# Optimization experiments

Hardware: AMD Instinct MI355X
Metric: run time of the kernel (lower is better)

The kernel has to match this reference:

```python
import jax, jax.numpy as jnp
import numpy as np

FACTOR = 1.0   # module's self.factor
EPS = 1e-6     # rmsnorm eps


def setup_inputs() -> dict:
    key = jax.random.key(0)
    k0, k1, k2, k3 = jax.random.split(key, 4)
    B, S = 4, 2048
    D_IN = D_STATE = D_OUT = 2048
    N_HEADS = 32
    HD = D_STATE // N_HEADS  # 64
    x = jax.random.normal(k0, (B, S, D_IN), jnp.float32)
    w_in = jax.random.normal(k1, (D_STATE, D_IN), jnp.float32) * 0.02
    b_in = jnp.zeros((D_STATE,), jnp.float32)
    state_weight = jax.random.normal(k2, (N_HEADS, HD, HD), jnp.float32) * 0.02
    norm_weight = jnp.ones((D_STATE,), jnp.float32)
    w_out = jax.random.normal(k3, (D_OUT, D_STATE), jnp.float32) * (0.02 / np.sqrt(2 * 24))
    return dict(x=x, w_in=w_in, b_in=b_in, state_weight=state_weight,
                norm_weight=norm_weight, w_out=w_out)


def _rnn_scan(xt, W):
    # xt: (B, S, N, H); W: (N, H, H)
    B, S, N, H = xt.shape

    def step(s, x_t):
        # s: (B, N, H) ; per-head linear recurrence with tanh nonlinearity
        s = jnp.tanh(jnp.einsum('bnh,nhk->bnk', s, W) + x_t)
        return s, s

    s0 = jnp.zeros((B, N, H), xt.dtype)
    _, states = jax.lax.scan(step, s0, jnp.swapaxes(xt, 0, 1))  # (S, B, N, H)
    return jnp.swapaxes(states, 0, 1)  # (B, S, N, H)


def reference(x, w_in, b_in, state_weight, norm_weight, w_out):
    B, S, _ = x.shape
    N, H, _ = state_weight.shape
    h = x @ w_in.T + b_in                      # input_projection: (B,S,state)
    h = h.reshape(B, S, N, H) * FACTOR
    W = state_weight * FACTOR
    states = _rnn_scan(h, W)                   # (B,S,N,H)
    y = states.reshape(B, S, N * H)
    # rmsnorm
    y = y * jax.lax.rsqrt(jnp.mean(y * y, axis=-1, keepdims=True) + EPS) * norm_weight
    return y @ w_out.T                         # output_projection (no bias)
```

## Files before the change

### kernel.cpp

```cpp
#include <hip/hip_runtime.h>
#include <hip/hip_bf16.h>
#include <cstdint>


typedef short bf16x8 __attribute__((ext_vector_type(8)));
typedef float f32x4 __attribute__((ext_vector_type(4)));
typedef _Float16 f16x2 __attribute__((ext_vector_type(2)));

#define GLD16(gp, lp)                                                          \
  __builtin_amdgcn_global_load_lds(                                            \
      (const __attribute__((address_space(1))) void*)(gp),                     \
      (__attribute__((address_space(3))) void*)(lp), 16, 0, 0)

__global__ __launch_bounds__(256) void cvt_f32_bf16(
    const float* __restrict__ in, __hip_bfloat16* __restrict__ out, int n4) {
  int i = blockIdx.x * 256 + threadIdx.x;
  if (i >= n4) return;
  float4 v = ((const float4*)in)[i];
  __hip_bfloat16 a = __float2bfloat16(v.x);
  __hip_bfloat16 b = __float2bfloat16(v.y);
  __hip_bfloat16 c = __float2bfloat16(v.z);
  __hip_bfloat16 d = __float2bfloat16(v.w);
  ushort4 p;
  p.x = *(unsigned short*)&a; p.y = *(unsigned short*)&b;
  p.z = *(unsigned short*)&c; p.w = *(unsigned short*)&d;
  ((ushort4*)out)[i] = p;
}

__global__ __launch_bounds__(256) void gemm_nt(
    const __hip_bfloat16* __restrict__ A, const __hip_bfloat16* __restrict__ B,
    const float* __restrict__ bias, float* __restrict__ C,
    int M, int N, int K) {
  __shared__ __hip_bfloat16 As[128 * 32];
  __shared__ __hip_bfloat16 Bs[128 * 32];
  const int tid  = threadIdx.x;
  const int lane = tid & 63;
  const int wave = tid >> 6;
  const int wm = wave >> 1, wn = wave & 1;

  const int id = blockIdx.y * gridDim.x + blockIdx.x;
  const int chunk = (gridDim.x * gridDim.y) >> 3;
  const int v = (id & 7) * chunk + (id >> 3);
  const int vbn = v / gridDim.y;
  const int vbm = v - vbn * gridDim.y;
  const long bm = (long)vbm * 128;
  const long bn = (long)vbn * 128;

  const int c0 = tid, c1 = tid + 256;
  const int r0 = c0 >> 2, k0 = (c0 & 3) * 8;
  const int r1 = c1 >> 2, k1 = (c1 & 3) * 8;
  __hip_bfloat16* lA0 = &As[(wave * 64) * 8];
  __hip_bfloat16* lA1 = &As[(256 + wave * 64) * 8];
  __hip_bfloat16* lB0 = &Bs[(wave * 64) * 8];
  __hip_bfloat16* lB1 = &Bs[(256 + wave * 64) * 8];
  const __hip_bfloat16* gA0 = A + (bm + r0) * (long)K + k0;
  const __hip_bfloat16* gA1 = A + (bm + r1) * (long)K + k1;
  const __hip_bfloat16* gB0 = B + (bn + r0) * (long)K + k0;
  const __hip_bfloat16* gB1 = B + (bn + r1) * (long)K + k1;

  const int fr = lane & 15;
  const int fk = (lane >> 4) * 8;

  f32x4 acc[4][4];
#pragma unroll
  for (int i = 0; i < 4; i++)
#pragma unroll
    for (int j = 0; j < 4; j++) acc[i][j] = {0.f, 0.f, 0.f, 0.f};

  for (int kt = 0; kt < K; kt += 32) {
    __syncthreads();
    GLD16(gA0 + kt, lA0);
    GLD16(gA1 + kt, lA1);
    GLD16(gB0 + kt, lB0);
    GLD16(gB1 + kt, lB1);
    __syncthreads();
    bf16x8 af[4], bfr[4];
#pragma unroll
    for (int t = 0; t < 4; t++)
      af[t] = *(const bf16x8*)&As[(wm * 64 + t * 16 + fr) * 32 + fk];
#pragma unroll
    for (int t = 0; t < 4; t++)
      bfr[t] = *(const bf16x8*)&Bs[(wn * 64 + t * 16 + fr) * 32 + fk];
#pragma unroll
    for (int i = 0; i < 4; i++)
#pragma unroll
      for (int j = 0; j < 4; j++)
        acc[i][j] = __builtin_amdgcn_mfma_f32_16x16x32_bf16(
            af[i], bfr[j], acc[i][j], 0, 0, 0);
  }

  const int cr = (lane >> 4) * 4;
  const int cc = lane & 15;
#pragma unroll
  for (int j = 0; j < 4; j++) {
    const long n = bn + wn * 64 + j * 16 + cc;
    const float bv = bias ? bias[n] : 0.0f;
#pragma unroll
    for (int i = 0; i < 4; i++) {
      const long m = bm + wm * 64 + i * 16 + cr;
#pragma unroll
      for (int r = 0; r < 4; r++)
        C[(m + r) * (long)N + n] = acc[i][j][r] + bv;
    }
  }
}

__device__ __forceinline__ float tanh_fast(float z) {
  float e = __builtin_amdgcn_exp2f(z * 2.8853900817779268f);
  return 1.0f - 2.0f * __builtin_amdgcn_rcpf(e + 1.0f);
}

__global__ __launch_bounds__(64) void scan_kernel(
    const float* __restrict__ Wst, float* __restrict__ h) {
  const int b = blockIdx.x >> 5;
  const int n = blockIdx.x & 31;
  const int lane = threadIdx.x;
  const float* Wn = Wst + n * 4096;

  f16x2 w2[32];
#pragma unroll
  for (int p = 0; p < 32; p++) {
    f16x2 t;
    t.x = (_Float16)Wn[(2 * p) * 64 + lane];
    t.y = (_Float16)Wn[(2 * p + 1) * 64 + lane];
    w2[p] = t;
  }

  __shared__ alignas(16) unsigned short s_h[64];

  int4 sv[8];
#pragma unroll
  for (int q = 0; q < 8; q++) sv[q] = make_int4(0, 0, 0, 0);

  float* hp = h + ((size_t)b * 2048) * 2048 + n * 64 + lane;
  float xcur[8], xnxt[8];
#pragma unroll
  for (int i = 0; i < 8; i++) xcur[i] = hp[(size_t)i * 2048];

  const f16x2 z2 = {(_Float16)0.f, (_Float16)0.f};

  for (int t0 = 0; t0 < 2048; t0 += 8) {
    if (t0 + 8 < 2048) {
#pragma unroll
      for (int i = 0; i < 8; i++)
        xnxt[i] = hp[(size_t)(t0 + 8 + i) * 2048];
    }
#pragma unroll
    for (int i = 0; i < 8; i++) {
      f16x2 ac0 = z2, ac1 = z2, ac2 = z2, ac3 = z2;
#pragma unroll
      for (int q = 0; q < 8; q++) {
        ac0 = __builtin_elementwise_fma(__builtin_bit_cast(f16x2, sv[q].x),
                                        w2[4 * q + 0], ac0);
        ac1 = __builtin_elementwise_fma(__builtin_bit_cast(f16x2, sv[q].y),
                                        w2[4 * q + 1], ac1);
        ac2 = __builtin_elementwise_fma(__builtin_bit_cast(f16x2, sv[q].z),
                                        w2[4 * q + 2], ac2);
        ac3 = __builtin_elementwise_fma(__builtin_bit_cast(f16x2, sv[q].w),
                                        w2[4 * q + 3], ac3);
      }
      f16x2 p01 = ac0 + ac1;
      f16x2 p23 = ac2 + ac3;
      f16x2 pt = p01 + p23;
      float z = (float)pt.x + (float)pt.y + xcur[i];
      float sn = tanh_fast(z);
      _Float16 sh = (_Float16)sn;
      s_h[lane] = __builtin_bit_cast(unsigned short, sh);
#pragma unroll
      for (int q = 0; q < 8; q++) sv[q] = ((const int4*)s_h)[q];
      hp[(size_t)(t0 + i) * 2048] = sn;
    }
#pragma unroll
    for (int i = 0; i < 8; i++) xcur[i] = xnxt[i];
  }
}

__global__ __launch_bounds__(256) void rmsnorm_to_bf16(
    const float* __restrict__ Y, const float* __restrict__ g,
    __hip_bfloat16* __restrict__ O) {
  const long row = blockIdx.x;
  const float* yr = Y + row * 2048;
  const int tid = threadIdx.x;
  float4 v0 = ((const float4*)yr)[tid * 2];
  float4 v1 = ((const float4*)yr)[tid * 2 + 1];
  float ss = v0.x * v0.x + v0.y * v0.y + v0.z * v0.z + v0.w * v0.w +
             v1.x * v1.x + v1.y * v1.y + v1.z * v1.z + v1.w * v1.w;
#pragma unroll
  for (int off = 32; off > 0; off >>= 1) ss += __shfl_down(ss, off);
  __shared__ float red[4];
  if ((tid & 63) == 0) red[tid >> 6] = ss;
  __syncthreads();
  float inv = rsqrtf((red[0] + red[1] + red[2] + red[3]) * (1.0f / 2048.0f)
                     + 1e-6f);
  float4 g0 = ((const float4*)(g + tid * 8))[0];
  float4 g1 = ((const float4*)(g + tid * 8))[1];
  float ov[8] = {v0.x * inv * g0.x, v0.y * inv * g0.y,
                 v0.z * inv * g0.z, v0.w * inv * g0.w,
                 v1.x * inv * g1.x, v1.y * inv * g1.y,
                 v1.z * inv * g1.z, v1.w * inv * g1.w};
  ushort4 p0, p1;
  __hip_bfloat16 t;
  t = __float2bfloat16(ov[0]); p0.x = *(unsigned short*)&t;
  t = __float2bfloat16(ov[1]); p0.y = *(unsigned short*)&t;
  t = __float2bfloat16(ov[2]); p0.z = *(unsigned short*)&t;
  t = __float2bfloat16(ov[3]); p0.w = *(unsigned short*)&t;
  t = __float2bfloat16(ov[4]); p1.x = *(unsigned short*)&t;
  t = __float2bfloat16(ov[5]); p1.y = *(unsigned short*)&t;
  t = __float2bfloat16(ov[6]); p1.z = *(unsigned short*)&t;
  t = __float2bfloat16(ov[7]); p1.w = *(unsigned short*)&t;
  ushort4* op = (ushort4*)(O + row * 2048 + tid * 8);
  op[0] = p0;
  op[1] = p1;
}

extern "C" void kernel_launch(void* const* d_in, const int* in_sizes, int n_in,
                              void* d_out, int out_size, void* d_ws,
                              size_t ws_size, hipStream_t stream) {
  const float* x     = (const float*)d_in[0];
  const float* w_in  = (const float*)d_in[1];
  const float* b_in  = (const float*)d_in[2];
  const float* w_st  = (const float*)d_in[3];
  const float* nw    = (const float*)d_in[4];
  const float* w_out = (const float*)d_in[5];
  float* out = (float*)d_out;

  char* ws = (char*)d_ws;
  __hip_bfloat16* x_bf  = (__hip_bfloat16*)(ws);
  __hip_bfloat16* wi_bf = (__hip_bfloat16*)(ws + 33554432);
  __hip_bfloat16* wo_bf = (__hip_bfloat16*)(ws + 41943040);
  float* h              = (float*)(ws + 50331648);

  cvt_f32_bf16<<<16384, 256, 0, stream>>>(x, x_bf, 4194304);
  cvt_f32_bf16<<<4096, 256, 0, stream>>>(w_in, wi_bf, 1048576);
  cvt_f32_bf16<<<4096, 256, 0, stream>>>(w_out, wo_bf, 1048576);

  gemm_nt<<<dim3(16, 64), 256, 0, stream>>>(x_bf, wi_bf, b_in, h,
                                            8192, 2048, 2048);
  scan_kernel<<<128, 64, 0, stream>>>(w_st, h);
  rmsnorm_to_bf16<<<8192, 256, 0, stream>>>(h, nw, x_bf);
  gemm_nt<<<dim3(16, 64), 256, 0, stream>>>(x_bf, wo_bf, nullptr, out,
                                            8192, 2048, 2048);
}
```

Baseline: 759.9 us.

## Use 256x256 GEMM tiles with double-buffered LDS and 512-thread blocks

Enlarges the GEMM block tile to 256x256 with eight waves, each computing a 128x64 sub-tile, which raises operand reuse per LDS load. It also adds a two-stage LDS buffer so the next K-slice is prefetched while MFMAs run on the current one. The grouped block-index swizzle is removed, and the grid shrinks to 256 blocks, which may reduce L2 locality and occupancy. Register pressure rises with 128 accumulator registers per lane.

```diff
diff --git a/kernel.cpp b/kernel.cpp
--- a/kernel.cpp
+++ b/kernel.cpp
@@ -27,67 +27,69 @@
   ((ushort4*)out)[i] = p;
 }
 
-__global__ __launch_bounds__(256) void gemm_nt(
+__global__ __launch_bounds__(512) void gemm_nt(
     const __hip_bfloat16* __restrict__ A, const __hip_bfloat16* __restrict__ B,
     const float* __restrict__ bias, float* __restrict__ C,
     int M, int N, int K) {
-  __shared__ __hip_bfloat16 As[128 * 32];
-  __shared__ __hip_bfloat16 Bs[128 * 32];
+  __shared__ __hip_bfloat16 As[2][256 * 32];
+  __shared__ __hip_bfloat16 Bs[2][256 * 32];
   const int tid  = threadIdx.x;
   const int lane = tid & 63;
   const int wave = tid >> 6;
-  const int wm = wave >> 1, wn = wave & 1;
-
-  const int id = blockIdx.y * gridDim.x + blockIdx.x;
-  const int chunk = (gridDim.x * gridDim.y) >> 3;
-  const int v = (id & 7) * chunk + (id >> 3);
-  const int vbn = v / gridDim.y;
-  const int vbm = v - vbn * gridDim.y;
-  const long bm = (long)vbm * 128;
-  const long bn = (long)vbn * 128;
-
-  const int c0 = tid, c1 = tid + 256;
-  const int r0 = c0 >> 2, k0 = (c0 & 3) * 8;
-  const int r1 = c1 >> 2, k1 = (c1 & 3) * 8;
-  __hip_bfloat16* lA0 = &As[(wave * 64) * 8];
-  __hip_bfloat16* lA1 = &As[(256 + wave * 64) * 8];
-  __hip_bfloat16* lB0 = &Bs[(wave * 64) * 8];
-  __hip_bfloat16* lB1 = &Bs[(256 + wave * 64) * 8];
+  const int wm = wave >> 2;
+  const int wn = wave & 3;
+  const long bm = (long)blockIdx.y * 256;
+  const long bn = (long)blockIdx.x * 256;
+
+  const int r0 = tid >> 2;
+  const int k0 = (tid & 3) * 8;
   const __hip_bfloat16* gA0 = A + (bm + r0) * (long)K + k0;
-  const __hip_bfloat16* gA1 = A + (bm + r1) * (long)K + k1;
+  const __hip_bfloat16* gA1 = A + (bm + 128 + r0) * (long)K + k0;
   const __hip_bfloat16* gB0 = B + (bn + r0) * (long)K + k0;
-  const __hip_bfloat16* gB1 = B + (bn + r1) * (long)K + k1;
+  const __hip_bfloat16* gB1 = B + (bn + 128 + r0) * (long)K + k0;
+
+#define STAGE(sbuf, kt)                                                        \
+  do {                                                                         \
+    GLD16(gA0 + (kt) * 32, &As[sbuf][wave * 512]);                             \
+    GLD16(gA1 + (kt) * 32, &As[sbuf][4096 + wave * 512]);                      \
+    GLD16(gB0 + (kt) * 32, &Bs[sbuf][wave * 512]);                             \
+    GLD16(gB1 + (kt) * 32, &Bs[sbuf][4096 + wave * 512]);                      \
+  } while (0)
 
   const int fr = lane & 15;
   const int fk = (lane >> 4) * 8;
 
-  f32x4 acc[4][4];
-#pragma unroll
-  for (int i = 0; i < 4; i++)
+  f32x4 acc[8][4];
+#pragma unroll
+  for (int i = 0; i < 8; i++)
 #pragma unroll
     for (int j = 0; j < 4; j++) acc[i][j] = {0.f, 0.f, 0.f, 0.f};
 
-  for (int kt = 0; kt < K; kt += 32) {
-    __syncthreads();
-    GLD16(gA0 + kt, lA0);
-    GLD16(gA1 + kt, lA1);
-    GLD16(gB0 + kt, lB0);
-    GLD16(gB1 + kt, lB1);
-    __syncthreads();
-    bf16x8 af[4], bfr[4];
+  STAGE(0, 0);
+  asm volatile("s_waitcnt vmcnt(0)" ::: "memory");
+  __syncthreads();
+
+  const int nk = K >> 5;
+  for (int kt = 0; kt < nk; kt++) {
+    const int cur = kt & 1;
+    if (kt + 1 < nk) STAGE(cur ^ 1, kt + 1);
+    bf16x8 af[8], bfr[4];
+#pragma unroll
+    for (int t = 0; t < 8; t++)
+      af[t] = *(const bf16x8*)&As[cur][(wm * 128 + t * 16 + fr) * 32 + fk];
 #pragma unroll
     for (int t = 0; t < 4; t++)
-      af[t] = *(const bf16x8*)&As[(wm * 64 + t * 16 + fr) * 32 + fk];
-#pragma unroll
-    for (int t = 0; t < 4; t++)
-      bfr[t] = *(const bf16x8*)&Bs[(wn * 64 + t * 16 + fr) * 32 + fk];
-#pragma unroll
-    for (int i = 0; i < 4; i++)
+      bfr[t] = *(const bf16x8*)&Bs[cur][(wn * 64 + t * 16 + fr) * 32 + fk];
+#pragma unroll
+    for (int i = 0; i < 8; i++)
 #pragma unroll
       for (int j = 0; j < 4; j++)
         acc[i][j] = __builtin_amdgcn_mfma_f32_16x16x32_bf16(
             af[i], bfr[j], acc[i][j], 0, 0, 0);
-  }
+    asm volatile("s_waitcnt vmcnt(0)" ::: "memory");
+    __syncthreads();
+  }
+#undef STAGE
 
   const int cr = (lane >> 4) * 4;
   const int cc = lane & 15;
@@ -96,8 +98,8 @@
     const long n = bn + wn * 64 + j * 16 + cc;
     const float bv = bias ? bias[n] : 0.0f;
 #pragma unroll
-    for (int i = 0; i < 4; i++) {
-      const long m = bm + wm * 64 + i * 16 + cr;
+    for (int i = 0; i < 8; i++) {
+      const long m = bm + wm * 128 + i * 16 + cr;
 #pragma unroll
       for (int r = 0; r < 4; r++)
         C[(m + r) * (long)N + n] = acc[i][j][r] + bv;
@@ -234,10 +236,10 @@
   cvt_f32_bf16<<<4096, 256, 0, stream>>>(w_in, wi_bf, 1048576);
   cvt_f32_bf16<<<4096, 256, 0, stream>>>(w_out, wo_bf, 1048576);
 
-  gemm_nt<<<dim3(16, 64), 256, 0, stream>>>(x_bf, wi_bf, b_in, h,
-                                            8192, 2048, 2048);
+  gemm_nt<<<dim3(8, 32), 512, 0, stream>>>(x_bf, wi_bf, b_in, h,
+                                           8192, 2048, 2048);
   scan_kernel<<<128, 64, 0, stream>>>(w_st, h);
   rmsnorm_to_bf16<<<8192, 256, 0, stream>>>(h, nw, x_bf);
-  gemm_nt<<<dim3(16, 64), 256, 0, stream>>>(x_bf, wo_bf, nullptr, out,
-                                            8192, 2048, 2048);
-}
+  gemm_nt<<<dim3(8, 32), 512, 0, stream>>>(x_bf, wo_bf, nullptr, out,
+                                           8192, 2048, 2048);
+}
```

New measurement: 718.8 us. -5.4%, faster.
